# Performance work log

Measured on AMD Instinct MI355X. Metric: run time of the kernel, lower is better.

## Reference

```python
import jax, jax.numpy as jnp
import numpy as np

B, S, D = 4, 2048, 768   # batch, seq_len, dim_inp
H, E = 12, 64            # num_heads, dim_out (per-head)
LN_EPS = 1e-5


def setup_inputs() -> dict:
    key = jax.random.key(0)
    ks = jax.random.split(key, 12)
    sd = 1.0 / np.sqrt(D)
    x = jax.random.normal(ks[0], (B, S, D), dtype=jnp.float32)
    Wq = jax.random.normal(ks[1], (H, D, E), dtype=jnp.float32) * sd
    bq = jax.random.normal(ks[2], (H, E), dtype=jnp.float32) * 0.02
    Wk = jax.random.normal(ks[3], (H, D, E), dtype=jnp.float32) * sd
    bk = jax.random.normal(ks[4], (H, E), dtype=jnp.float32) * 0.02
    Wv = jax.random.normal(ks[5], (H, D, E), dtype=jnp.float32) * sd
    bv = jax.random.normal(ks[6], (H, E), dtype=jnp.float32) * 0.02
    Wo = jax.random.normal(ks[7], (H * E, D), dtype=jnp.float32) * (1.0 / np.sqrt(H * E))
    bo = jax.random.normal(ks[8], (D,), dtype=jnp.float32) * 0.02
    gamma = jnp.ones((D,), dtype=jnp.float32)
    beta = jnp.zeros((D,), dtype=jnp.float32)
    return {"input_tensor": x, "Wq": Wq, "bq": bq, "Wk": Wk, "bk": bk,
            "Wv": Wv, "bv": bv, "Wo": Wo, "bo": bo, "gamma": gamma, "beta": beta}


def reference(input_tensor, Wq, bq, Wk, bk, Wv, bv, Wo, bo, gamma, beta):
    x = input_tensor  # [B,S,D]
    # all heads at once: [B,H,S,E]
    q = jnp.einsum('bsd,hde->bhse', x, Wq) + bq[None, :, None, :]
    k = jnp.einsum('bsd,hde->bhse', x, Wk) + bk[None, :, None, :]
    v = jnp.einsum('bsd,hde->bhse', x, Wv) + bv[None, :, None, :]
    # NOTE: original divides by sqrt(seq_len) (query.size(1)), not sqrt(head_dim)
    scale = jnp.sqrt(jnp.float32(q.shape[2]))
    scores = jnp.einsum('bhse,bhte->bhst', q, k) / scale  # [B,H,S,S]
    attn = jax.nn.softmax(scores, axis=-1)
    ctx = jnp.einsum('bhst,bhte->bhse', attn, v)          # [B,H,S,E]
    # concat heads along last dim: [B,S,H*E]
    ctx = ctx.transpose(0, 2, 1, 3).reshape(x.shape[0], x.shape[1], -1)
    proj = ctx @ Wo + bo                                   # [B,S,D]
    h = x + proj
    mu = jnp.mean(h, axis=-1, keepdims=True)
    var = jnp.mean(jnp.square(h - mu), axis=-1, keepdims=True)
    y = (h - mu) * jax.lax.rsqrt(var + LN_EPS) * gamma + beta
    return y
```

## Files before the change

### kernel.cpp

```cpp
#include <hip/hip_runtime.h>


typedef __bf16 bf16x8 __attribute__((ext_vector_type(8)));
typedef __bf16 bf16x4 __attribute__((ext_vector_type(4)));
typedef float  f32x4  __attribute__((ext_vector_type(4)));
typedef float  f32x16 __attribute__((ext_vector_type(16)));
typedef unsigned u32x4 __attribute__((ext_vector_type(4)));

#define MFMA16(a,b,c) __builtin_amdgcn_mfma_f32_16x16x32_bf16((a),(b),(c),0,0,0)
#define MFMA32(a,b,c) __builtin_amdgcn_mfma_f32_32x32x16_bf16((a),(b),(c),0,0,0)
#define QSCALE2 (0.022097086912079612f * 1.4426950408889634f)

__device__ __forceinline__ void gload16(const void* g, void* l) {
  __builtin_amdgcn_global_load_lds((const __attribute__((address_space(1))) void*)g,
                                   (__attribute__((address_space(3))) void*)l, 16, 0, 0);
}

__global__ __launch_bounds__(256) void pack_kernel(
    const float* __restrict__ x, const float* __restrict__ Wq,
    const float* __restrict__ Wk, const float* __restrict__ Wv,
    const float* __restrict__ Wo,
    __bf16* __restrict__ xb, __bf16* __restrict__ wqkv, __bf16* __restrict__ wot) {
  int tid = blockIdx.x * 256 + threadIdx.x;
  int nth = gridDim.x * 256;
  for (int i = tid; i < 8192 * 768 / 4; i += nth) {
    float4 v = ((const float4*)x)[i];
    bf16x4 o; o[0] = (__bf16)v.x; o[1] = (__bf16)v.y; o[2] = (__bf16)v.z; o[3] = (__bf16)v.w;
    ((bf16x4*)xb)[i] = o;
  }
  for (int i = tid; i < 3 * 768 * 768; i += nth) {
    int n = i / 768, d = i - n * 768;
    int p = n / 768;
    int wn = n - p * 768;
    int h = wn >> 6, e = wn & 63;
    const float* W = (p == 0) ? Wq : (p == 1) ? Wk : Wv;
    wqkv[i] = (__bf16)W[(h * 768 + d) * 64 + e];
  }
  for (int i = tid; i < 768 * 768; i += nth) {
    int n = i / 768, k = i - n * 768;
    wot[i] = (__bf16)Wo[k * 768 + n];
  }
}

#define GEMM_CORE(A_, Bt_, m0_, n0_)                                              \
  __shared__ __bf16 As[128 * 32];                                                 \
  __shared__ __bf16 Bs[128 * 32];                                                 \
  const int tid = threadIdx.x;                                                    \
  const int w = tid >> 6, lane = tid & 63, ln = lane & 15, hi = lane >> 4;        \
  const int wr = w >> 1, wc = w & 1;                                              \
  f32x4 acc[4][4];                                                                \
  {                                                                               \
    f32x4 z = {0.f, 0.f, 0.f, 0.f};                                               \
    _Pragma("unroll") for (int i = 0; i < 4; ++i)                                 \
      _Pragma("unroll") for (int j = 0; j < 4; ++j) acc[i][j] = z;                \
  }                                                                               \
  {                                                                               \
    const int r0 = tid >> 2, cc = (tid & 3) * 8;                                  \
    const __bf16* ga0 = A_ + (size_t)(m0_ + r0) * 768 + cc;                       \
    const __bf16* ga1 = A_ + (size_t)(m0_ + 64 + r0) * 768 + cc;                  \
    const __bf16* gb0 = Bt_ + (size_t)(n0_ + r0) * 768 + cc;                      \
    const __bf16* gb1 = Bt_ + (size_t)(n0_ + 64 + r0) * 768 + cc;                 \
    __bf16* la0 = &As[w * 512];                                                   \
    __bf16* la1 = &As[2048 + w * 512];                                            \
    __bf16* lb0 = &Bs[w * 512];                                                   \
    __bf16* lb1 = &Bs[2048 + w * 512];                                            \
    for (int kt = 0; kt < 24; ++kt) {                                             \
      const int kk = kt * 32;                                                     \
      gload16(ga0 + kk, la0);                                                     \
      gload16(ga1 + kk, la1);                                                     \
      gload16(gb0 + kk, lb0);                                                     \
      gload16(gb1 + kk, lb1);                                                     \
      __syncthreads();                                                            \
      bf16x8 af[4], bfv[4];                                                       \
      _Pragma("unroll") for (int mt = 0; mt < 4; ++mt)                            \
        af[mt] = *(const bf16x8*)&As[(wr * 64 + mt * 16 + ln) * 32 + hi * 8];     \
      _Pragma("unroll") for (int nt = 0; nt < 4; ++nt)                            \
        bfv[nt] = *(const bf16x8*)&Bs[(wc * 64 + nt * 16 + ln) * 32 + hi * 8];    \
      _Pragma("unroll") for (int mt = 0; mt < 4; ++mt)                            \
        _Pragma("unroll") for (int nt = 0; nt < 4; ++nt)                          \
          acc[mt][nt] = MFMA16(af[mt], bfv[nt], acc[mt][nt]);                     \
      __syncthreads();                                                            \
    }                                                                             \
  }

__global__ __launch_bounds__(256) void gemm_qkv(
    const __bf16* __restrict__ A, const __bf16* __restrict__ Bt,
    const float* __restrict__ bq, const float* __restrict__ bk,
    const float* __restrict__ bv,
    __bf16* __restrict__ qb, __bf16* __restrict__ kb, __bf16* __restrict__ vt) {
  const int m0 = blockIdx.y * 128, n0 = blockIdx.x * 128;
  GEMM_CORE(A, Bt, m0, n0)
  const int p = n0 / 768;
  const float* bias = (p == 0) ? bq : (p == 1) ? bk : bv;
  const float sc = (p == 0) ? QSCALE2 : 1.0f;
#pragma unroll
  for (int nt = 0; nt < 4; ++nt) {
    int n = n0 + wc * 64 + nt * 16 + ln;
    int wn = n - p * 768;
    int h = wn >> 6, e = wn & 63;
    float bb = bias[wn];
#pragma unroll
    for (int mt = 0; mt < 4; ++mt) {
      int mrow = m0 + wr * 64 + mt * 16 + hi * 4;
      int b = mrow >> 11, s0 = mrow & 2047;
      if (p == 2) {
        bf16x4 pk;
#pragma unroll
        for (int r = 0; r < 4; ++r) pk[r] = (__bf16)(acc[mt][nt][r] + bb);
        *(bf16x4*)&vt[(((size_t)b * 12 + h) * 64 + e) * 2048 + s0] = pk;
      } else {
        __bf16* dst = (p == 0) ? qb : kb;
#pragma unroll
        for (int r = 0; r < 4; ++r)
          dst[(((size_t)b * 12 + h) * 2048 + s0 + r) * 64 + e] =
              (__bf16)((acc[mt][nt][r] + bb) * sc);
      }
    }
  }
}

__global__ __launch_bounds__(256) void gemm_proj(
    const __bf16* __restrict__ A, const __bf16* __restrict__ Bt,
    const float* __restrict__ bo, const float* __restrict__ xres,
    float* __restrict__ hout) {
  const int m0 = blockIdx.y * 128, n0 = blockIdx.x * 128;
  GEMM_CORE(A, Bt, m0, n0)
#pragma unroll
  for (int nt = 0; nt < 4; ++nt) {
    int n = n0 + wc * 64 + nt * 16 + ln;
    float bb = bo[n];
#pragma unroll
    for (int mt = 0; mt < 4; ++mt) {
      int mrow = m0 + wr * 64 + mt * 16 + hi * 4;
#pragma unroll
      for (int r = 0; r < 4; ++r) {
        size_t idx = (size_t)(mrow + r) * 768 + n;
        hout[idx] = acc[mt][nt][r] + bb + xres[idx];
      }
    }
  }
}

__global__ __launch_bounds__(256) void attn_kernel(
    const __bf16* __restrict__ qb, const __bf16* __restrict__ kb,
    const __bf16* __restrict__ vt, __bf16* __restrict__ ctx) {
  __shared__ __align__(16) char lds[32768];
  const int tid = threadIdx.x;
  const int w = tid >> 6, lane = tid & 63;
  const int l31 = lane & 31, h = lane >> 5;
  const int bh = blockIdx.x;
  const int q0 = blockIdx.y * 128 + w * 32;

  const int o0 = tid * 16, o1 = o0 + 4096;
  const int r0s = o0 >> 7, cb0 = o0 & 127;
  const int r1s = o1 >> 7, cb1 = o1 & 127;
  const char* kgb = (const char*)(kb + (size_t)bh * 2048 * 64);
  const char* vgb = (const char*)(vt + (size_t)bh * 64 * 2048);
  const char* ksrc0 = kgb + r0s * 128 + (cb0 ^ ((r0s & 7) << 4));
  const char* ksrc1 = kgb + r1s * 128 + (cb1 ^ ((r1s & 7) << 4));
  const char* vsrc0 = vgb + r0s * 4096 + (cb0 ^ ((r0s & 7) << 4));
  const char* vsrc1 = vgb + r1s * 4096 + (cb1 ^ ((r1s & 7) << 4));
  char* kl0 = lds + w * 1024;
  char* vl0 = lds + 16384 + w * 1024;

#define STAGE(t_, b_) do {                                   \
    gload16(ksrc0 + (size_t)(t_) * 8192, kl0 + (b_) * 8192); \
    gload16(ksrc1 + (size_t)(t_) * 8192, kl0 + (b_) * 8192 + 4096); \
    gload16(vsrc0 + (size_t)(t_) * 128,  vl0 + (b_) * 8192); \
    gload16(vsrc1 + (size_t)(t_) * 128,  vl0 + (b_) * 8192 + 4096); \
  } while (0)

  const __bf16* qp = qb + ((size_t)bh * 2048 + q0 + l31) * 64 + h * 8;
  bf16x8 qf[4];
#pragma unroll
  for (int s = 0; s < 4; ++s) qf[s] = *(const bf16x8*)(qp + 16 * s);

  const int swz = (l31 & 7) << 4;
  const int krd = l31 * 128 + ((h * 16) ^ swz);
  const int vrd = 16384 + l31 * 128 + ((h * 16) ^ swz);

  float lsum = 0.f;
  f32x16 cacc[2];
#pragma unroll
  for (int et = 0; et < 2; ++et)
#pragma unroll
    for (int r = 0; r < 16; ++r) cacc[et][r] = 0.f;

  STAGE(0, 0);
  __syncthreads();
  int buf = 0;

  for (int t = 0; t < 32; ++t) {
    if (t < 31) STAGE(t + 1, buf ^ 1);
    const char* kb_l = lds + buf * 8192;
    u32x4 pau[4];
#pragma unroll
    for (int kvt = 0; kvt < 2; ++kvt) {
      f32x16 sa;
#pragma unroll
      for (int r = 0; r < 16; ++r) sa[r] = 0.f;
      __builtin_amdgcn_s_setprio(1);
#pragma unroll
      for (int s = 0; s < 4; ++s) {
        bf16x8 ka = *(const bf16x8*)(kb_l + ((krd + kvt * 4096) ^ (s * 32)));
        sa = MFMA32(ka, qf[s], sa);
      }
      __builtin_amdgcn_s_setprio(0);
      unsigned c0, c1, c2, c3, c4, c5, c6, c7;
#define PKPAIR(dst_, i_)                                                     \
      {                                                                      \
        float pa_ = __builtin_amdgcn_exp2f(sa[2 * (i_)]);                    \
        float pb_ = __builtin_amdgcn_exp2f(sa[2 * (i_) + 1]);                \
        lsum += pa_ + pb_;                                                   \
        asm("v_cvt_pk_bf16_f32 %0, %1, %2" : "=v"(dst_) : "v"(pa_), "v"(pb_)); \
      }
      PKPAIR(c0, 0) PKPAIR(c1, 1) PKPAIR(c2, 2) PKPAIR(c3, 3)
      PKPAIR(c4, 4) PKPAIR(c5, 5) PKPAIR(c6, 6) PKPAIR(c7, 7)
#undef PKPAIR
      asm("v_permlane32_swap_b32 %0, %1" : "+v"(c0), "+v"(c2));
      asm("v_permlane32_swap_b32 %0, %1" : "+v"(c1), "+v"(c3));
      asm("v_permlane32_swap_b32 %0, %1" : "+v"(c4), "+v"(c6));
      asm("v_permlane32_swap_b32 %0, %1" : "+v"(c5), "+v"(c7));
      pau[2 * kvt][0] = c0; pau[2 * kvt][1] = c1;
      pau[2 * kvt][2] = c2; pau[2 * kvt][3] = c3;
      pau[2 * kvt + 1][0] = c4; pau[2 * kvt + 1][1] = c5;
      pau[2 * kvt + 1][2] = c6; pau[2 * kvt + 1][3] = c7;
    }
    const char* vb_l = lds + buf * 8192;
    __builtin_amdgcn_s_setprio(1);
#pragma unroll
    for (int ks = 0; ks < 4; ++ks) {
      bf16x8 paf = __builtin_bit_cast(bf16x8, pau[ks]);
      bf16x8 bv0 = *(const bf16x8*)(vb_l + ((vrd + 0 * 4096) ^ (ks * 32)));
      bf16x8 bv1 = *(const bf16x8*)(vb_l + ((vrd + 1 * 4096) ^ (ks * 32)));
      cacc[0] = MFMA32(paf, bv0, cacc[0]);
      cacc[1] = MFMA32(paf, bv1, cacc[1]);
    }
    __builtin_amdgcn_s_setprio(0);
    __syncthreads();
    buf ^= 1;
  }
#undef STAGE

  lsum += __shfl_xor(lsum, 32, 64);
  float inv = 1.0f / lsum;
  const int b = bh / 12, hh = bh - b * 12;
#pragma unroll
  for (int r = 0; r < 16; ++r) {
    const int ql = (r & 3) + 8 * (r >> 2) + 4 * h;
    float rl = __shfl(inv, ql, 64);
    size_t base = ((size_t)b * 2048 + q0 + ql) * 768 + hh * 64 + l31;
    ctx[base]      = (__bf16)(cacc[0][r] * rl);
    ctx[base + 32] = (__bf16)(cacc[1][r] * rl);
  }
}

__global__ __launch_bounds__(256) void ln_kernel(
    const float* __restrict__ hb, const float* __restrict__ gamma,
    const float* __restrict__ beta, float* __restrict__ out) {
  __shared__ float ssum[4], ssq[4];
  const int row = blockIdx.x, t = threadIdx.x;
  const float* hr = hb + (size_t)row * 768;
  float v0 = hr[t], v1 = hr[t + 256], v2 = hr[t + 512];
  float sum = v0 + v1 + v2;
  float sq = v0 * v0 + v1 * v1 + v2 * v2;
#pragma unroll
  for (int mask = 1; mask < 64; mask <<= 1) {
    sum += __shfl_xor(sum, mask, 64);
    sq += __shfl_xor(sq, mask, 64);
  }
  const int w = t >> 6;
  if ((t & 63) == 0) { ssum[w] = sum; ssq[w] = sq; }
  __syncthreads();
  float s1 = ssum[0] + ssum[1] + ssum[2] + ssum[3];
  float s2 = ssq[0] + ssq[1] + ssq[2] + ssq[3];
  float mu = s1 * (1.0f / 768.0f);
  float var = s2 * (1.0f / 768.0f) - mu * mu;
  float rs = rsqrtf(var + 1e-5f);
  float* orow = out + (size_t)row * 768;
  orow[t]       = (v0 - mu) * rs * gamma[t]       + beta[t];
  orow[t + 256] = (v1 - mu) * rs * gamma[t + 256] + beta[t + 256];
  orow[t + 512] = (v2 - mu) * rs * gamma[t + 512] + beta[t + 512];
}

extern "C" void kernel_launch(void* const* d_in, const int* in_sizes, int n_in,
                              void* d_out, int out_size, void* d_ws, size_t ws_size,
                              hipStream_t stream) {
  const float* x     = (const float*)d_in[0];
  const float* Wq    = (const float*)d_in[1];
  const float* bq    = (const float*)d_in[2];
  const float* Wk    = (const float*)d_in[3];
  const float* bk    = (const float*)d_in[4];
  const float* Wv    = (const float*)d_in[5];
  const float* bv    = (const float*)d_in[6];
  const float* Wo    = (const float*)d_in[7];
  const float* bo    = (const float*)d_in[8];
  const float* gamma = (const float*)d_in[9];
  const float* beta  = (const float*)d_in[10];
  float* out = (float*)d_out;

  char* ws = (char*)d_ws;
  __bf16* xb   = (__bf16*)(ws);
  __bf16* wqkv = (__bf16*)(ws + 12582912);
  __bf16* wot  = (__bf16*)(ws + 16121856);
  __bf16* qb   = (__bf16*)(ws + 17301504);
  __bf16* kb   = (__bf16*)(ws + 29884416);
  __bf16* vt   = (__bf16*)(ws + 42467328);
  __bf16* ctx  = (__bf16*)(ws + 55050240);
  float*  hb   = (float*)(ws + 67633152);

  pack_kernel<<<dim3(1024), dim3(256), 0, stream>>>(x, Wq, Wk, Wv, Wo, xb, wqkv, wot);
  gemm_qkv<<<dim3(18, 64), dim3(256), 0, stream>>>(xb, wqkv, bq, bk, bv, qb, kb, vt);
  attn_kernel<<<dim3(48, 16), dim3(256), 0, stream>>>(qb, kb, vt, ctx);
  gemm_proj<<<dim3(6, 64), dim3(256), 0, stream>>>(ctx, wot, bo, x, hb);
  ln_kernel<<<dim3(8192), dim3(256), 0, stream>>>(hb, gamma, beta, out);
}
```

Measured before the change: 172.9 us.

## Swizzle block order in GEMMs and attention, preload K/V fragments, split row sums

```diff
diff --git a/kernel.cpp b/kernel.cpp
--- a/kernel.cpp
+++ b/kernel.cpp
@@ -88,7 +88,9 @@
     const float* __restrict__ bq, const float* __restrict__ bk,
     const float* __restrict__ bv,
     __bf16* __restrict__ qb, __bf16* __restrict__ kb, __bf16* __restrict__ vt) {
-  const int m0 = blockIdx.y * 128, n0 = blockIdx.x * 128;
+  const int lin = blockIdx.y * 18 + blockIdx.x;
+  const int swzb = (lin & 7) * 144 + (lin >> 3);
+  const int m0 = (swzb / 18) * 128, n0 = (swzb % 18) * 128;
   GEMM_CORE(A, Bt, m0, n0)
   const int p = n0 / 768;
   const float* bias = (p == 0) ? bq : (p == 1) ? bk : bv;
@@ -123,7 +125,9 @@
     const __bf16* __restrict__ A, const __bf16* __restrict__ Bt,
     const float* __restrict__ bo, const float* __restrict__ xres,
     float* __restrict__ hout) {
-  const int m0 = blockIdx.y * 128, n0 = blockIdx.x * 128;
+  const int lin = blockIdx.y * 6 + blockIdx.x;
+  const int swzb = (lin & 7) * 48 + (lin >> 3);
+  const int m0 = (swzb / 6) * 128, n0 = (swzb % 6) * 128;
   GEMM_CORE(A, Bt, m0, n0)
 #pragma unroll
   for (int nt = 0; nt < 4; ++nt) {
@@ -141,15 +145,17 @@
   }
 }
 
-__global__ __launch_bounds__(256) void attn_kernel(
+__global__ __launch_bounds__(256, 3) void attn_kernel(
     const __bf16* __restrict__ qb, const __bf16* __restrict__ kb,
     const __bf16* __restrict__ vt, __bf16* __restrict__ ctx) {
   __shared__ __align__(16) char lds[32768];
   const int tid = threadIdx.x;
   const int w = tid >> 6, lane = tid & 63;
   const int l31 = lane & 31, h = lane >> 5;
-  const int bh = blockIdx.x;
-  const int q0 = blockIdx.y * 128 + w * 32;
+  const int lin = blockIdx.x * 16 + blockIdx.y;
+  const int swzb = (lin & 7) * 96 + (lin >> 3);
+  const int bh = swzb >> 4;
+  const int q0 = (swzb & 15) * 128 + w * 32;
 
   const int o0 = tid * 16, o1 = o0 + 4096;
   const int r0s = o0 >> 7, cb0 = o0 & 127;
@@ -179,7 +185,7 @@
   const int krd = l31 * 128 + ((h * 16) ^ swz);
   const int vrd = 16384 + l31 * 128 + ((h * 16) ^ swz);
 
-  float lsum = 0.f;
+  float ls0 = 0.f, ls1 = 0.f, ls2 = 0.f, ls3 = 0.f;
   f32x16 cacc[2];
 #pragma unroll
   for (int et = 0; et < 2; ++et)
@@ -193,6 +199,17 @@
   for (int t = 0; t < 32; ++t) {
     if (t < 31) STAGE(t + 1, buf ^ 1);
     const char* kb_l = lds + buf * 8192;
+    bf16x8 kf[2][4], vf[4][2];
+#pragma unroll
+    for (int kvt = 0; kvt < 2; ++kvt)
+#pragma unroll
+      for (int s = 0; s < 4; ++s)
+        kf[kvt][s] = *(const bf16x8*)(kb_l + ((krd + kvt * 4096) ^ (s * 32)));
+#pragma unroll
+    for (int ks = 0; ks < 4; ++ks) {
+      vf[ks][0] = *(const bf16x8*)(kb_l + ((vrd + 0 * 4096) ^ (ks * 32)));
+      vf[ks][1] = *(const bf16x8*)(kb_l + ((vrd + 1 * 4096) ^ (ks * 32)));
+    }
     u32x4 pau[4];
 #pragma unroll
     for (int kvt = 0; kvt < 2; ++kvt) {
@@ -201,21 +218,18 @@
       for (int r = 0; r < 16; ++r) sa[r] = 0.f;
       __builtin_amdgcn_s_setprio(1);
 #pragma unroll
-      for (int s = 0; s < 4; ++s) {
-        bf16x8 ka = *(const bf16x8*)(kb_l + ((krd + kvt * 4096) ^ (s * 32)));
-        sa = MFMA32(ka, qf[s], sa);
-      }
+      for (int s = 0; s < 4; ++s) sa = MFMA32(kf[kvt][s], qf[s], sa);
       __builtin_amdgcn_s_setprio(0);
       unsigned c0, c1, c2, c3, c4, c5, c6, c7;
-#define PKPAIR(dst_, i_)                                                     \
+#define PKPAIR(dst_, i_, ls_)                                                \
       {                                                                      \
         float pa_ = __builtin_amdgcn_exp2f(sa[2 * (i_)]);                    \
         float pb_ = __builtin_amdgcn_exp2f(sa[2 * (i_) + 1]);                \
-        lsum += pa_ + pb_;                                                   \
+        ls_ += pa_ + pb_;                                                    \
         asm("v_cvt_pk_bf16_f32 %0, %1, %2" : "=v"(dst_) : "v"(pa_), "v"(pb_)); \
       }
-      PKPAIR(c0, 0) PKPAIR(c1, 1) PKPAIR(c2, 2) PKPAIR(c3, 3)
-      PKPAIR(c4, 4) PKPAIR(c5, 5) PKPAIR(c6, 6) PKPAIR(c7, 7)
+      PKPAIR(c0, 0, ls0) PKPAIR(c1, 1, ls1) PKPAIR(c2, 2, ls2) PKPAIR(c3, 3, ls3)
+      PKPAIR(c4, 4, ls0) PKPAIR(c5, 5, ls1) PKPAIR(c6, 6, ls2) PKPAIR(c7, 7, ls3)
 #undef PKPAIR
       asm("v_permlane32_swap_b32 %0, %1" : "+v"(c0), "+v"(c2));
       asm("v_permlane32_swap_b32 %0, %1" : "+v"(c1), "+v"(c3));
@@ -226,15 +240,12 @@
       pau[2 * kvt + 1][0] = c4; pau[2 * kvt + 1][1] = c5;
       pau[2 * kvt + 1][2] = c6; pau[2 * kvt + 1][3] = c7;
     }
-    const char* vb_l = lds + buf * 8192;
     __builtin_amdgcn_s_setprio(1);
 #pragma unroll
     for (int ks = 0; ks < 4; ++ks) {
       bf16x8 paf = __builtin_bit_cast(bf16x8, pau[ks]);
-      bf16x8 bv0 = *(const bf16x8*)(vb_l + ((vrd + 0 * 4096) ^ (ks * 32)));
-      bf16x8 bv1 = *(const bf16x8*)(vb_l + ((vrd + 1 * 4096) ^ (ks * 32)));
-      cacc[0] = MFMA32(paf, bv0, cacc[0]);
-      cacc[1] = MFMA32(paf, bv1, cacc[1]);
+      cacc[0] = MFMA32(paf, vf[ks][0], cacc[0]);
+      cacc[1] = MFMA32(paf, vf[ks][1], cacc[1]);
     }
     __builtin_amdgcn_s_setprio(0);
     __syncthreads();
@@ -242,6 +253,7 @@
   }
 #undef STAGE
 
+  float lsum = (ls0 + ls1) + (ls2 + ls3);
   lsum += __shfl_xor(lsum, 32, 64);
   float inv = 1.0f / lsum;
   const int b = bh / 12, hh = bh - b * 12;
```

New measurement: 170.2 us. About the same (-1.6%).
